# Kernel tuning notes

Measured on AMD Instinct MI355X. Metric: run time of the kernel, lower is better.

Reference implementation:

```python
import jax, jax.numpy as jnp
import numpy as np

MOMENTUM = 0.9
NUM_CLASSES = 10000
BANK_DIM = 1024
BATCH = 4096


def setup_inputs() -> dict:
    key = jax.random.key(0)
    k1, k2, k3, k4 = jax.random.split(key, 4)
    scores = jax.random.normal(k1, (BATCH, NUM_CLASSES), dtype=jnp.float32)
    feat = jax.random.normal(k2, (BATCH, BANK_DIM), dtype=jnp.float32)
    update_feat_bank = jax.random.normal(k3, (NUM_CLASSES, BANK_DIM), dtype=jnp.float32)
    update_times = jnp.zeros((NUM_CLASSES,), dtype=jnp.float32)
    labels = jax.random.randint(k4, (BATCH,), 0, NUM_CLASSES, dtype=jnp.int64 if jax.config.read('jax_enable_x64') else jnp.int32)
    return {"scores": scores, "feat": feat, "update_feat_bank": update_feat_bank,
            "update_times": update_times, "labels": labels}


def reference(scores, feat, update_feat_bank, update_times, labels):
    """Faithful vectorization of AvgMem.proc with choose='err'.

    Original (sequential, per chosen sample i in batch order):
        bank[l_i] = m * bank[l_i] + (1 - m) * feat[i];  times[l_i] += 1
    Closed form per label l with chosen samples i1<...<ik:
        bank[l] = m^k * bank0[l] + (1-m) * sum_j m^(k-j) feat[i_j]
    i.e. each sample's weight is (1-m) * m^(#later chosen samples with same label).
    """
    m = jnp.float32(MOMENTUM)
    C = update_feat_bank.shape[0]
    B = labels.shape[0]

    # softmax is monotonic -> argmax of softmax(scores) == argmax of scores
    pred = jnp.argmax(scores, axis=1)
    chosen = pred != labels  # choose == 'err'

    # c[i] = number of later chosen samples with the same label (BxB pairwise)
    same = labels[:, None] == labels[None, :]
    later = jnp.arange(B)[None, :] > jnp.arange(B)[:, None]
    c = jnp.sum(same & later & chosen[None, :], axis=1).astype(feat.dtype)

    w = jnp.where(chosen, (1.0 - m) * m ** c, 0.0).astype(feat.dtype)  # [B]

    delta = jax.ops.segment_sum(w[:, None] * feat, labels, num_segments=C)  # [C, D]
    k = jax.ops.segment_sum(chosen.astype(update_times.dtype), labels, num_segments=C)  # [C]

    new_bank = (m ** k)[:, None] * update_feat_bank + delta
    new_times = update_times + k
    return new_bank, new_times
```

## Files before the change

### kernel.cpp

```cpp
#include <hip/hip_runtime.h>

#define MOM 0.9f
#define ONE_MINUS_MOM 0.1f
#define MAXK 16

__global__ __launch_bounds__(256) void argmax_key_kernel(
    const float* __restrict__ scores, const int* __restrict__ labels,
    int* __restrict__ key, int* __restrict__ cnt, int C)
{
    if (threadIdx.x < 4) {
        int l = (blockIdx.x << 2) | threadIdx.x;
        if (l < C) cnt[l] = 0;
    }

    const int row = blockIdx.x;
    const float* rp = scores + (size_t)row * C;
    float best = -__builtin_inff();
    int bidx = 0x7fffffff;

    const int nv = C >> 2;
    const float4* r4 = (const float4*)rp;
    for (int v = threadIdx.x; v < nv; v += 256) {
        float4 s = r4[v];
        int b = v << 2;
        if (s.x > best) { best = s.x; bidx = b; }
        if (s.y > best) { best = s.y; bidx = b + 1; }
        if (s.z > best) { best = s.z; bidx = b + 2; }
        if (s.w > best) { best = s.w; bidx = b + 3; }
    }
    for (int c = (nv << 2) + threadIdx.x; c < C; c += 256) {
        float s = rp[c];
        if (s > best) { best = s; bidx = c; }
    }

    #pragma unroll
    for (int off = 32; off > 0; off >>= 1) {
        float ov = __shfl_xor(best, off);
        int   oi = __shfl_xor(bidx, off);
        if (ov > best || (ov == best && oi < bidx)) { best = ov; bidx = oi; }
    }

    __shared__ float sv[4];
    __shared__ int   si[4];
    const int lane = threadIdx.x & 63;
    const int wid  = threadIdx.x >> 6;
    if (lane == 0) { sv[wid] = best; si[wid] = bidx; }
    __syncthreads();
    if (threadIdx.x == 0) {
        float bv = sv[0]; int bi = si[0];
        #pragma unroll
        for (int w = 1; w < 4; ++w) {
            float ov = sv[w]; int oi = si[w];
            if (ov > bv || (ov == bv && oi < bi)) { bv = ov; bi = oi; }
        }
        int lab = labels[row];
        key[row] = (lab << 1) | ((bi != lab) ? 1 : 0);
    }
}

__global__ __launch_bounds__(256) void rank_kernel(
    const int* __restrict__ key, int* __restrict__ cnt,
    int* __restrict__ slot, int B)
{
    const int lane = threadIdx.x & 63;
    const int i = blockIdx.x * 4 + (threadIdx.x >> 6);
    if (i >= B) return;
    const int mykey = key[i];
    if (!(mykey & 1)) return;

    int e = 0, c = 0;
    for (int base = 0; base < B; base += 64) {
        int j = base + lane;
        int kj = (j < B) ? key[j] : -1;
        bool match = (kj == mykey);
        e += __popcll(__ballot(match && (j < i)));
        c += __popcll(__ballot(match && (j > i)));
    }
    if (lane == 0) {
        int l = mykey >> 1;
        if (e < MAXK) slot[l * MAXK + e] = i;
        if (e == 0) cnt[l] = c + 1;
    }
}

__global__ __launch_bounds__(256) void update_kernel(
    const float* __restrict__ bank, const float* __restrict__ times,
    const float* __restrict__ feat, const int* __restrict__ cnt,
    const int* __restrict__ slot,
    float* __restrict__ out_bank, float* __restrict__ out_times, int C, int D)
{
    const int lane = threadIdx.x & 63;
    const int wid  = threadIdx.x >> 6;
    const int l = (blockIdx.x << 2) | wid;
    if (l >= C) return;

    const int k = cnt[l];
    const int kk = (k < MAXK) ? k : MAXK;
    float scale = 1.0f;
    for (int p = 0; p < k; ++p) scale *= MOM;

    const float4* brow = (const float4*)(bank + (size_t)l * D);
    float4* orow = (float4*)(out_bank + (size_t)l * D);
    const int sbase = l * MAXK;
    const int nv = D >> 2;

    if (nv == 256) {
        float4 a0 = brow[lane];
        float4 a1 = brow[lane + 64];
        float4 a2 = brow[lane + 128];
        float4 a3 = brow[lane + 192];
        a0.x *= scale; a0.y *= scale; a0.z *= scale; a0.w *= scale;
        a1.x *= scale; a1.y *= scale; a1.z *= scale; a1.w *= scale;
        a2.x *= scale; a2.y *= scale; a2.z *= scale; a2.w *= scale;
        a3.x *= scale; a3.y *= scale; a3.z *= scale; a3.w *= scale;
        float wgt = ONE_MINUS_MOM;
        for (int r = kk - 1; r >= 0; --r) {
            int j = slot[sbase + r];
            const float4* f4 = (const float4*)(feat + (size_t)j * D);
            float4 f0 = f4[lane];
            float4 f1 = f4[lane + 64];
            float4 f2 = f4[lane + 128];
            float4 f3 = f4[lane + 192];
            a0.x += wgt * f0.x; a0.y += wgt * f0.y; a0.z += wgt * f0.z; a0.w += wgt * f0.w;
            a1.x += wgt * f1.x; a1.y += wgt * f1.y; a1.z += wgt * f1.z; a1.w += wgt * f1.w;
            a2.x += wgt * f2.x; a2.y += wgt * f2.y; a2.z += wgt * f2.z; a2.w += wgt * f2.w;
            a3.x += wgt * f3.x; a3.y += wgt * f3.y; a3.z += wgt * f3.z; a3.w += wgt * f3.w;
            wgt *= MOM;
        }
        orow[lane] = a0;
        orow[lane + 64] = a1;
        orow[lane + 128] = a2;
        orow[lane + 192] = a3;
    } else {
        for (int v = lane; v < nv; v += 64) {
            float4 a = brow[v];
            a.x *= scale; a.y *= scale; a.z *= scale; a.w *= scale;
            float wgt = ONE_MINUS_MOM;
            for (int r = kk - 1; r >= 0; --r) {
                int j = slot[sbase + r];
                const float4* f4 = (const float4*)(feat + (size_t)j * D);
                float4 f = f4[v];
                a.x += wgt * f.x; a.y += wgt * f.y; a.z += wgt * f.z; a.w += wgt * f.w;
                wgt *= MOM;
            }
            orow[v] = a;
        }
    }
    if (lane == 0) out_times[l] = times[l] + (float)k;
}

extern "C" void kernel_launch(void* const* d_in, const int* in_sizes, int n_in,
                              void* d_out, int out_size, void* d_ws, size_t ws_size,
                              hipStream_t stream) {
    const float* scores = (const float*)d_in[0];
    const float* feat   = (const float*)d_in[1];
    const float* bank   = (const float*)d_in[2];
    const float* times  = (const float*)d_in[3];
    const int*   labels = (const int*)d_in[4];

    const int B = in_sizes[4];
    const int C = in_sizes[3];
    const int D = in_sizes[1] / B;

    float* out_bank  = (float*)d_out;
    float* out_times = out_bank + (size_t)C * D;

    int* key  = (int*)d_ws;
    int* cnt  = key + B;
    int* slot = cnt + C;

    argmax_key_kernel<<<B, 256, 0, stream>>>(scores, labels, key, cnt, C);
    rank_kernel<<<(B + 3) / 4, 256, 0, stream>>>(key, cnt, slot, B);
    update_kernel<<<(C + 3) / 4, 256, 0, stream>>>(bank, times, feat, cnt, slot,
                                                   out_bank, out_times, C, D);
}
```

Before: 61.75 us.

## Overlap bank copy with argmax and skip untouched rows in update

Extra blocks are added to the argmax launch so it also copies the bank and times to the output. The update kernel then returns early for labels with zero chosen samples, which avoids a dependent re-read and write of most bank rows after the rank stage. The argmax loop now keeps four independent per-component maxima to shorten the compare dependency chain. In exchange, rows that do get updated are written twice, and the copy competes with the scores read for bandwidth.

```diff
diff --git a/kernel.cpp b/kernel.cpp
--- a/kernel.cpp
+++ b/kernel.cpp
@@ -4,30 +4,50 @@
 #define ONE_MINUS_MOM 0.1f
 #define MAXK 16
 
-__global__ __launch_bounds__(256) void argmax_key_kernel(
+__global__ __launch_bounds__(256) void fused_argmax_copy_kernel(
     const float* __restrict__ scores, const int* __restrict__ labels,
-    int* __restrict__ key, int* __restrict__ cnt, int C)
+    const float* __restrict__ bank, const float* __restrict__ times,
+    int* __restrict__ key, int* __restrict__ cnt,
+    float* __restrict__ out_bank, float* __restrict__ out_times,
+    int B, int C, int D)
 {
+    if ((int)blockIdx.x >= B) {
+        const int cb = blockIdx.x - B;
+        const int lane = threadIdx.x & 63;
+        const int wid  = threadIdx.x >> 6;
+        const int l = (cb << 2) | wid;
+        if (l >= C) return;
+        const float4* brow = (const float4*)(bank + (size_t)l * D);
+        float4* orow = (float4*)(out_bank + (size_t)l * D);
+        const int nv = D >> 2;
+        for (int v = lane; v < nv; v += 64) orow[v] = brow[v];
+        if (lane == 0) out_times[l] = times[l];
+        return;
+    }
+
     if (threadIdx.x < 4) {
-        int l = (blockIdx.x << 2) | threadIdx.x;
+        int l = ((int)blockIdx.x << 2) | (int)threadIdx.x;
         if (l < C) cnt[l] = 0;
     }
 
     const int row = blockIdx.x;
     const float* rp = scores + (size_t)row * C;
-    float best = -__builtin_inff();
-    int bidx = 0x7fffffff;
-
     const int nv = C >> 2;
     const float4* r4 = (const float4*)rp;
+
+    float b0 = -__builtin_inff(), b1 = b0, b2 = b0, b3 = b0;
+    int v0 = 0x7fffffff, v1 = v0, v2 = v0, v3 = v0;
     for (int v = threadIdx.x; v < nv; v += 256) {
         float4 s = r4[v];
-        int b = v << 2;
-        if (s.x > best) { best = s.x; bidx = b; }
-        if (s.y > best) { best = s.y; bidx = b + 1; }
-        if (s.z > best) { best = s.z; bidx = b + 2; }
-        if (s.w > best) { best = s.w; bidx = b + 3; }
+        if (s.x > b0) { b0 = s.x; v0 = v; }
+        if (s.y > b1) { b1 = s.y; v1 = v; }
+        if (s.z > b2) { b2 = s.z; v2 = v; }
+        if (s.w > b3) { b3 = s.w; v3 = v; }
     }
+    float best = b0; int bidx = (v0 << 2) | 0;
+    { int oi = (v1 << 2) | 1; if (b1 > best || (b1 == best && oi < bidx)) { best = b1; bidx = oi; } }
+    { int oi = (v2 << 2) | 2; if (b2 > best || (b2 == best && oi < bidx)) { best = b2; bidx = oi; } }
+    { int oi = (v3 << 2) | 3; if (b3 > best || (b3 == best && oi < bidx)) { best = b3; bidx = oi; } }
     for (int c = (nv << 2) + threadIdx.x; c < C; c += 256) {
         float s = rp[c];
         if (s > best) { best = s; bidx = c; }
@@ -95,6 +115,7 @@
     if (l >= C) return;
 
     const int k = cnt[l];
+    if (k == 0) return;
     const int kk = (k < MAXK) ? k : MAXK;
     float scale = 1.0f;
     for (int p = 0; p < k; ++p) scale *= MOM;
@@ -169,7 +190,9 @@
     int* cnt  = key + B;
     int* slot = cnt + C;
 
-    argmax_key_kernel<<<B, 256, 0, stream>>>(scores, labels, key, cnt, C);
+    const int copy_blocks = (C + 3) / 4;
+    fused_argmax_copy_kernel<<<B + copy_blocks, 256, 0, stream>>>(
+        scores, labels, bank, times, key, cnt, out_bank, out_times, B, C, D);
     rank_kernel<<<(B + 3) / 4, 256, 0, stream>>>(key, cnt, slot, B);
     update_kernel<<<(C + 3) / 4, 256, 0, stream>>>(bank, times, feat, cnt, slot,
                                                    out_bank, out_times, C, D);
```

Result: slower. 66.38 us (+7.5%).
